# Kernel tuning notes

Measured on AMD Instinct MI355X. Metric: run time of the kernel, lower is better.

The kernel has to match this reference:

```python
import jax, jax.numpy as jnp
import numpy as np

N_NODES = 50000
N_EDGES = 800000
IN_DIM = 256
OUT_DIM = 64


def setup_inputs() -> dict:
    key = jax.random.key(0)
    k1, k2, k3, k4, k5 = jax.random.split(key, 5)
    h = jax.random.normal(k1, (N_NODES, IN_DIM), dtype=jnp.float32)
    # fc: Linear(in_dim, out_dim, bias=False) -> weight shape [out_dim, in_dim]
    W_fc = jax.random.normal(k2, (OUT_DIM, IN_DIM), dtype=jnp.float32) / np.sqrt(IN_DIM)
    # attn_fc: Linear(2*out_dim, 1, bias=False) -> weight shape [1, 2*out_dim]
    W_attn = jax.random.normal(k3, (1, 2 * OUT_DIM), dtype=jnp.float32) / np.sqrt(2 * OUT_DIM)
    src = jax.random.randint(k4, (N_EDGES,), 0, N_NODES, dtype=jnp.int64 if jax.config.read('jax_enable_x64') else jnp.int32).astype(jnp.int32)
    dst = jax.random.randint(k5, (N_EDGES,), 0, N_NODES, dtype=jnp.int32)
    return {"h": h, "W_fc": W_fc, "W_attn": W_attn, "src": src, "dst": dst}


def reference(h, W_fc, W_attn, src, dst):
    # z = self.fc(h)
    z = h @ W_fc.T                              # [N, D]
    # edge_attention: e = leaky_relu(attn_fc(cat(z_src, z_dst)))
    z_src = z[src]                              # [E, D] gather
    z_dst = z[dst]                              # [E, D] gather
    z2 = jnp.concatenate([z_src, z_dst], axis=1)  # [E, 2D]
    e = jax.nn.leaky_relu(z2 @ W_attn.T)[:, 0]  # [E], torch default slope 0.01
    # reduce_func: segment softmax over incoming edges per dst node
    n = h.shape[0]
    m = jax.ops.segment_max(e, dst, num_segments=n)        # [N] per-node max
    e_exp = jnp.exp(e - m[dst])                             # [E] stable exp
    denom = jax.ops.segment_sum(e_exp, dst, num_segments=n)  # [N]
    alpha = e_exp / jnp.maximum(denom, 1e-16)[dst]          # [E]
    # h' = sum_j alpha_ij * z_j
    out = jax.ops.segment_sum(alpha[:, None] * z_src, dst, num_segments=n)  # [N, D]
    return out
```

## Files before the change

kernel.cpp:

```cpp
#include <hip/hip_runtime.h>

#define N_NODES 50000
#define N_EDGES 800000
#define IN_DIM  256
#define OUT_DIM 64
#define BINW    128
#define NBINS   512
#define NBINS_USED ((N_NODES + BINW - 1) / BINW)
#define PB      112
#define CH4     ((N_EDGES / 4 + PB - 1) / PB)
#define NB_GEMM ((N_NODES + 63) / 64)
#define GRID_FUSED 896

typedef _Float16 f16;
typedef __attribute__((ext_vector_type(2))) __fp16 hf16x2;
typedef __attribute__((ext_vector_type(4))) _Float16 f16x4;
typedef __attribute__((ext_vector_type(8))) _Float16 f16x8;
typedef __attribute__((ext_vector_type(4))) float f32x4;

__device__ __forceinline__ unsigned int pack_sw(int s, float w) {
    f16 hw = (f16)w;
    unsigned short us;
    __builtin_memcpy(&us, &hw, 2);
    return ((unsigned int)s << 16) | us;
}
__device__ __forceinline__ float unpack_w(unsigned int e) {
    unsigned short us = (unsigned short)(e & 0xffffu);
    f16 hw;
    __builtin_memcpy(&hw, &us, 2);
    return (float)hw;
}


__global__ __launch_bounds__(256) void k_prep(const float* __restrict__ W,
                                              f16* __restrict__ Wh,
                                              int* __restrict__ binCount) {
    int idx = blockIdx.x * 256 + threadIdx.x;
    if (idx < (OUT_DIM * IN_DIM) / 4) {
        float4 v = ((const float4*)W)[idx];
        f16x4 p = { (f16)v.x, (f16)v.y, (f16)v.z, (f16)v.w };
        ((f16x4*)Wh)[idx] = p;
    }
    if (idx < NBINS) binCount[idx] = 0;
}

__global__ __launch_bounds__(256) void k_fused(const float* __restrict__ h,
                                               const f16* __restrict__ Wh,
                                               const float* __restrict__ Wa,
                                               const int* __restrict__ dst,
                                               f16* __restrict__ z,
                                               float* __restrict__ a_src,
                                               float* __restrict__ a_dst,
                                               int* __restrict__ binCount,
                                               int* __restrict__ base) {
    __shared__ int hist[NBINS];
    const int g = blockIdx.x;
    const int t = threadIdx.x;

    if ((g & 7) == 7) {
        const int pb = g >> 3;
        for (int b = t; b < NBINS; b += 256) hist[b] = 0;
        __syncthreads();
        const int s4 = pb * CH4;
        const int e4 = min(s4 + CH4, N_EDGES / 4);
        for (int i4 = s4 + t; i4 < e4; i4 += 256) {
            int4 dv = ((const int4*)dst)[i4];
            atomicAdd(&hist[dv.x >> 7], 1);
            atomicAdd(&hist[dv.y >> 7], 1);
            atomicAdd(&hist[dv.z >> 7], 1);
            atomicAdd(&hist[dv.w >> 7], 1);
        }
        __syncthreads();
        for (int b = t; b < NBINS; b += 256) {
            int c = hist[b];
            if (c) base[pb * NBINS + b] = atomicAdd(&binCount[b], c);
        }
        return;
    }

    const int gemm_id = g - (g >> 3);
    if (gemm_id >= NB_GEMM) return;

    const int row0  = gemm_id * 64;
    const int lane  = t & 63;
    const int wid   = t >> 6;
    const int cl    = lane & 15;
    const int khalf = lane >> 4;

    int arow = row0 + wid * 16 + cl;
    if (arow >= N_NODES) arow = N_NODES - 1;
    const float* hrow = h + (size_t)arow * IN_DIM;

    f32x4 acc[4] = {};

    #pragma unroll 4
    for (int kc = 0; kc < IN_DIM; kc += 32) {
        const int k0 = kc + khalf * 8;
        float4 va = *(const float4*)&hrow[k0];
        float4 vb = *(const float4*)&hrow[k0 + 4];
        union { hf16x2 h2[4]; f16x8 h8; } ua;
        ua.h2[0] = __builtin_amdgcn_cvt_pkrtz(va.x, va.y);
        ua.h2[1] = __builtin_amdgcn_cvt_pkrtz(va.z, va.w);
        ua.h2[2] = __builtin_amdgcn_cvt_pkrtz(vb.x, vb.y);
        ua.h2[3] = __builtin_amdgcn_cvt_pkrtz(vb.z, vb.w);
        f16x8 a = ua.h8;
        #pragma unroll
        for (int ct = 0; ct < 4; ++ct) {
            const int col = ct * 16 + cl;
            f16x8 b = *(const f16x8*)&Wh[col * 256 + k0];
            acc[ct] = __builtin_amdgcn_mfma_f32_16x16x32_f16(a, b, acc[ct], 0, 0, 0);
        }
    }

    const int rbase = row0 + wid * 16 + khalf * 4;
    #pragma unroll
    for (int ct = 0; ct < 4; ++ct) {
        #pragma unroll
        for (int r = 0; r < 4; ++r) {
            int row = rbase + r;
            if (row < N_NODES)
                z[(size_t)row * OUT_DIM + ct * 16 + cl] = (f16)acc[ct][r];
        }
    }

    float wa1[4], wa2[4];
    #pragma unroll
    for (int ct = 0; ct < 4; ++ct) {
        wa1[ct] = Wa[ct * 16 + cl];
        wa2[ct] = Wa[64 + ct * 16 + cl];
    }
    #pragma unroll
    for (int r = 0; r < 4; ++r) {
        float s1 = 0.f, s2 = 0.f;
        #pragma unroll
        for (int ct = 0; ct < 4; ++ct) {
            s1 += acc[ct][r] * wa1[ct];
            s2 += acc[ct][r] * wa2[ct];
        }
        #pragma unroll
        for (int off = 1; off < 16; off <<= 1) {
            s1 += __shfl_xor(s1, off);
            s2 += __shfl_xor(s2, off);
        }
        int row = rbase + r;
        if (cl == 0 && row < N_NODES) {
            a_src[row] = s1;
            a_dst[row] = s2;
        }
    }
}

__global__ __launch_bounds__(256) void k_place(const int* __restrict__ src,
                                               const int* __restrict__ dst,
                                               const int* __restrict__ binCount,
                                               const int* __restrict__ base,
                                               int* __restrict__ ebuf) {
    __shared__ int cursor[NBINS];
    const int pb = blockIdx.x;
    const int t  = threadIdx.x;

    if (t < 64) {
        int vals[8]; int run = 0;
        #pragma unroll
        for (int i = 0; i < 8; ++i) { int c = binCount[t * 8 + i]; vals[i] = run; run += c; }
        int incl = run;
        #pragma unroll
        for (int off = 1; off < 64; off <<= 1) {
            int u = __shfl_up(incl, off);
            if (t >= off) incl += u;
        }
        const int lex = incl - run;
        #pragma unroll
        for (int i = 0; i < 8; ++i) cursor[t * 8 + i] = lex + vals[i];
    }
    __syncthreads();
    for (int b = t; b < NBINS; b += 256) cursor[b] += base[pb * NBINS + b];
    __syncthreads();

    const int s4 = pb * CH4;
    const int e4 = min(s4 + CH4, N_EDGES / 4);
    for (int i4 = s4 + t; i4 < e4; i4 += 256) {
        int4 dv = ((const int4*)dst)[i4];
        int4 sv = ((const int4*)src)[i4];
        int slot;
        slot = atomicAdd(&cursor[dv.x >> 7], 1); ebuf[slot] = (sv.x << 7) | (dv.x & 127);
        slot = atomicAdd(&cursor[dv.y >> 7], 1); ebuf[slot] = (sv.y << 7) | (dv.y & 127);
        slot = atomicAdd(&cursor[dv.z >> 7], 1); ebuf[slot] = (sv.z << 7) | (dv.z & 127);
        slot = atomicAdd(&cursor[dv.w >> 7], 1); ebuf[slot] = (sv.w << 7) | (dv.w & 127);
    }
}

__global__ __launch_bounds__(256) void k_place2(const int* __restrict__ ebuf,
                                                const int* __restrict__ binCount,
                                                const float* __restrict__ a_src,
                                                const float* __restrict__ a_dst,
                                                int* __restrict__ csr,
                                                int* __restrict__ rowptr) {
    __shared__ int cnt[BINW];
    __shared__ int cur[BINW];
    __shared__ float adl[BINW];
    __shared__ int sh_estart;
    const int b  = blockIdx.x;
    const int t  = threadIdx.x;
    const int node0 = b * BINW;
    const int ecnt  = binCount[b];

    if (t < 64) {
        int partial = 0;
        for (int i = t; i < b; i += 64) partial += binCount[i];
        #pragma unroll
        for (int off = 32; off; off >>= 1) partial += __shfl_xor(partial, off);
        if (t == 0) sh_estart = partial;
    }
    if (t < BINW) {
        cnt[t] = 0;
        int gd = node0 + t;
        adl[t] = (gd < N_NODES) ? a_dst[gd] : 0.f;
    }
    __syncthreads();
    const int estart = sh_estart;

    for (int i = t; i < ecnt; i += 256)
        atomicAdd(&cnt[ebuf[estart + i] & (BINW - 1)], 1);
    __syncthreads();

    if (t < 64) {
        int v0 = cnt[t], v1 = cnt[t + 64];
        int i0 = v0;
        #pragma unroll
        for (int off = 1; off < 64; off <<= 1) {
            int u = __shfl_up(i0, off);
            if (t >= off) i0 += u;
        }
        int tot0 = __shfl(i0, 63);
        int i1 = v1;
        #pragma unroll
        for (int off = 1; off < 64; off <<= 1) {
            int u = __shfl_up(i1, off);
            if (t >= off) i1 += u;
        }
        int e0 = i0 - v0;
        int e1 = tot0 + i1 - v1;
        cur[t]      = e0;
        cur[t + 64] = e1;
        if (node0 + t <= N_NODES)      rowptr[node0 + t]      = estart + e0;
        if (node0 + t + 64 <= N_NODES) rowptr[node0 + t + 64] = estart + e1;
    }
    __syncthreads();

    for (int i = t; i < ecnt; i += 256) {
        int pk = ebuf[estart + i];
        int ld = pk & (BINW - 1);
        int s  = pk >> 7;
        float u = a_src[s] + adl[ld];
        u = u > 0.f ? u : 0.01f * u;
        float w = __expf(u);
        int p  = atomicAdd(&cur[ld], 1);
        csr[estart + p] = (int)pack_sw(s, w);
    }
}

__global__ __launch_bounds__(256) void k_aggregate(const int* __restrict__ rowptr,
                                                   const int* __restrict__ csr,
                                                   const float* __restrict__ a_src,
                                                   const float* __restrict__ a_dst,
                                                   const f16* __restrict__ z,
                                                   float* __restrict__ out) {
    __shared__ unsigned int buf[4][64];
    const int wid  = threadIdx.x >> 6;
    const int lane = threadIdx.x & 63;
    const int node = blockIdx.x * 4 + wid;
    if (node >= N_NODES) return;

    const int beg = rowptr[node];
    const int end = rowptr[node + 1];
    const int deg = end - beg;

    const int grp = lane >> 3;
    const int cl  = lane & 7;
    float dn = 0.0f;
    float acc8[8] = {0.f, 0.f, 0.f, 0.f, 0.f, 0.f, 0.f, 0.f};

    if (deg <= 64) {
        unsigned int e = 0;
        if (lane < deg) e = (unsigned int)csr[beg + lane];
        dn = unpack_w(e);

        buf[wid][lane] = e;
        __builtin_amdgcn_wave_barrier();

        const int kmax = (deg + 7) & ~7;
        for (int k = 0; k < kmax; k += 8) {
            unsigned int pe = buf[wid][k + grp];
            int   sk = (int)(pe >> 16);
            float wk = unpack_w(pe);
            f16x8 zv = *(const f16x8*)&z[(size_t)sk * OUT_DIM + cl * 8];
            #pragma unroll
            for (int j = 0; j < 8; ++j)
                acc8[j] = fmaf(wk, (float)zv[j], acc8[j]);
        }
    } else {
        const float adst = a_dst[node];
        float mx = -INFINITY;
        for (int j = beg + lane; j < end; j += 64) {
            int s = (int)(((unsigned int)csr[j]) >> 16);
            float u = a_src[s] + adst;
            u = u > 0.0f ? u : 0.01f * u;
            mx = fmaxf(mx, u);
        }
        #pragma unroll
        for (int off = 32; off; off >>= 1) mx = fmaxf(mx, __shfl_xor(mx, off));

        for (int base_ = beg; base_ < end; base_ += 64) {
            int rem = end - base_; if (rem > 64) rem = 64;
            int s = 0; float w = 0.0f;
            if (lane < rem) {
                s = (int)(((unsigned int)csr[base_ + lane]) >> 16);
                float u = a_src[s] + adst;
                u = u > 0.0f ? u : 0.01f * u;
                w = __expf(u - mx);
            }
            dn += w;
            __builtin_amdgcn_wave_barrier();
            buf[wid][lane] = pack_sw(s, w);
            __builtin_amdgcn_wave_barrier();

            const int kmax = (rem + 7) & ~7;
            for (int k = 0; k < kmax; k += 8) {
                unsigned int pe = buf[wid][k + grp];
                int   sk = (int)(pe >> 16);
                float wk = unpack_w(pe);
                f16x8 zv = *(const f16x8*)&z[(size_t)sk * OUT_DIM + cl * 8];
                #pragma unroll
                for (int j = 0; j < 8; ++j)
                    acc8[j] = fmaf(wk, (float)zv[j], acc8[j]);
            }
            __builtin_amdgcn_wave_barrier();
        }
    }

    #pragma unroll
    for (int off = 32; off; off >>= 1) dn += __shfl_xor(dn, off);
    #pragma unroll
    for (int off = 8; off < 64; off <<= 1) {
        #pragma unroll
        for (int j = 0; j < 8; ++j)
            acc8[j] += __shfl_xor(acc8[j], off);
    }

    if (lane < 8) {
        float inv = 1.0f / fmaxf(dn, 1e-16f);
        float4 o0 = make_float4(acc8[0] * inv, acc8[1] * inv, acc8[2] * inv, acc8[3] * inv);
        float4 o1 = make_float4(acc8[4] * inv, acc8[5] * inv, acc8[6] * inv, acc8[7] * inv);
        *(float4*)&out[(size_t)node * OUT_DIM + lane * 8]     = o0;
        *(float4*)&out[(size_t)node * OUT_DIM + lane * 8 + 4] = o1;
    }
}


extern "C" void kernel_launch(void* const* d_in, const int* in_sizes, int n_in,
                              void* d_out, int out_size, void* d_ws, size_t ws_size,
                              hipStream_t stream) {
    const float* h      = (const float*)d_in[0];
    const float* W_fc   = (const float*)d_in[1];
    const float* W_attn = (const float*)d_in[2];
    const int*   src    = (const int*)d_in[3];
    const int*   dst    = (const int*)d_in[4];
    float* out = (float*)d_out;

    f16*   z        = (f16*)d_ws;
    f16*   Wh       = z + (size_t)N_NODES * OUT_DIM;
    float* a_src    = (float*)(Wh + OUT_DIM * IN_DIM);
    float* a_dst    = a_src + N_NODES;
    int*   binCount = (int*)(a_dst + N_NODES);
    int*   rowptr   = binCount + NBINS;
    int*   base     = rowptr + (N_NODES + 1);
    int*   ebuf     = base + PB * NBINS;
    int*   csr      = ebuf + N_EDGES;

    k_prep<<<16, 256, 0, stream>>>(W_fc, Wh, binCount);
    k_fused<<<GRID_FUSED, 256, 0, stream>>>(h, Wh, W_attn, dst, z, a_src, a_dst, binCount, base);
    k_place<<<PB, 256, 0, stream>>>(src, dst, binCount, base, ebuf);
    k_place2<<<NBINS_USED, 256, 0, stream>>>(ebuf, binCount, a_src, a_dst, csr, rowptr);
    k_aggregate<<<(N_NODES + 3) / 4, 256, 0, stream>>>(rowptr, csr, a_src, a_dst, z, out);
}
```

Before: 80.03 us.

## Drop prep kernel: convert weights inline and derive bin offsets from per-block histograms

Removes the k_prep launch. The GEMM now reads fp32 weights directly and converts them to fp16 in registers. The global binCount atomics are replaced by per-block histogram writes, and k_place recomputes per-bin totals and prefix offsets by summing all block histograms, then publishes bin start and total arrays for k_place2. This saves one kernel launch and the atomics, at the cost of redundant weight conversion in every GEMM block and each place block reading 112x512 histogram entries.

Result: slower. 95.31 us (+19.1%).

```diff
diff --git a/kernel.cpp b/kernel.cpp
--- a/kernel.cpp
+++ b/kernel.cpp
@@ -32,26 +32,13 @@
 }
 
 
-__global__ __launch_bounds__(256) void k_prep(const float* __restrict__ W,
-                                              f16* __restrict__ Wh,
-                                              int* __restrict__ binCount) {
-    int idx = blockIdx.x * 256 + threadIdx.x;
-    if (idx < (OUT_DIM * IN_DIM) / 4) {
-        float4 v = ((const float4*)W)[idx];
-        f16x4 p = { (f16)v.x, (f16)v.y, (f16)v.z, (f16)v.w };
-        ((f16x4*)Wh)[idx] = p;
-    }
-    if (idx < NBINS) binCount[idx] = 0;
-}
-
 __global__ __launch_bounds__(256) void k_fused(const float* __restrict__ h,
-                                               const f16* __restrict__ Wh,
+                                               const float* __restrict__ W,
                                                const float* __restrict__ Wa,
                                                const int* __restrict__ dst,
                                                f16* __restrict__ z,
                                                float* __restrict__ a_src,
                                                float* __restrict__ a_dst,
-                                               int* __restrict__ binCount,
                                                int* __restrict__ base) {
     __shared__ int hist[NBINS];
     const int g = blockIdx.x;
@@ -71,10 +58,8 @@
             atomicAdd(&hist[dv.w >> 7], 1);
         }
         __syncthreads();
-        for (int b = t; b < NBINS; b += 256) {
-            int c = hist[b];
-            if (c) base[pb * NBINS + b] = atomicAdd(&binCount[b], c);
-        }
+        for (int b = t; b < NBINS; b += 256)
+            base[pb * NBINS + b] = hist[b];
         return;
     }
 
@@ -107,8 +92,15 @@
         #pragma unroll
         for (int ct = 0; ct < 4; ++ct) {
             const int col = ct * 16 + cl;
-            f16x8 b = *(const f16x8*)&Wh[col * 256 + k0];
-            acc[ct] = __builtin_amdgcn_mfma_f32_16x16x32_f16(a, b, acc[ct], 0, 0, 0);
+            const float* wrow = W + (size_t)col * IN_DIM;
+            float4 wa4 = *(const float4*)&wrow[k0];
+            float4 wb4 = *(const float4*)&wrow[k0 + 4];
+            union { hf16x2 h2[4]; f16x8 h8; } ub;
+            ub.h2[0] = __builtin_amdgcn_cvt_pkrtz(wa4.x, wa4.y);
+            ub.h2[1] = __builtin_amdgcn_cvt_pkrtz(wa4.z, wa4.w);
+            ub.h2[2] = __builtin_amdgcn_cvt_pkrtz(wb4.x, wb4.y);
+            ub.h2[3] = __builtin_amdgcn_cvt_pkrtz(wb4.z, wb4.w);
+            acc[ct] = __builtin_amdgcn_mfma_f32_16x16x32_f16(a, ub.h8, acc[ct], 0, 0, 0);
         }
     }
 
@@ -152,17 +144,34 @@
 
 __global__ __launch_bounds__(256) void k_place(const int* __restrict__ src,
                                                const int* __restrict__ dst,
-                                               const int* __restrict__ binCount,
                                                const int* __restrict__ base,
+                                               int* __restrict__ binStartG,
+                                               int* __restrict__ binTotalG,
                                                int* __restrict__ ebuf) {
     __shared__ int cursor[NBINS];
+    __shared__ int totalL[NBINS];
+    __shared__ int bstart[NBINS];
     const int pb = blockIdx.x;
     const int t  = threadIdx.x;
 
+    int myPre[2];
+    #pragma unroll
+    for (int i = 0; i < 2; ++i) {
+        const int b = t + i * 256;
+        int total = 0, pre = 0;
+        for (int q = 0; q < PB; ++q) {
+            int v = base[q * NBINS + b];
+            total += v;
+            if (q < pb) pre += v;
+        }
+        totalL[b] = total;
+        myPre[i] = pre;
+    }
+    __syncthreads();
     if (t < 64) {
         int vals[8]; int run = 0;
         #pragma unroll
-        for (int i = 0; i < 8; ++i) { int c = binCount[t * 8 + i]; vals[i] = run; run += c; }
+        for (int i = 0; i < 8; ++i) { int c = totalL[t * 8 + i]; vals[i] = run; run += c; }
         int incl = run;
         #pragma unroll
         for (int off = 1; off < 64; off <<= 1) {
@@ -171,10 +180,18 @@
         }
         const int lex = incl - run;
         #pragma unroll
-        for (int i = 0; i < 8; ++i) cursor[t * 8 + i] = lex + vals[i];
-    }
-    __syncthreads();
-    for (int b = t; b < NBINS; b += 256) cursor[b] += base[pb * NBINS + b];
+        for (int i = 0; i < 8; ++i) bstart[t * 8 + i] = lex + vals[i];
+    }
+    __syncthreads();
+    #pragma unroll
+    for (int i = 0; i < 2; ++i) {
+        const int b = t + i * 256;
+        cursor[b] = bstart[b] + myPre[i];
+        if (pb == 0) {
+            binStartG[b] = bstart[b];
+            binTotalG[b] = totalL[b];
+        }
+    }
     __syncthreads();
 
     const int s4 = pb * CH4;
@@ -191,7 +208,8 @@
 }
 
 __global__ __launch_bounds__(256) void k_place2(const int* __restrict__ ebuf,
-                                                const int* __restrict__ binCount,
+                                                const int* __restrict__ binStartG,
+                                                const int* __restrict__ binTotalG,
                                                 const float* __restrict__ a_src,
                                                 const float* __restrict__ a_dst,
                                                 int* __restrict__ csr,
@@ -199,26 +217,18 @@
     __shared__ int cnt[BINW];
     __shared__ int cur[BINW];
     __shared__ float adl[BINW];
-    __shared__ int sh_estart;
     const int b  = blockIdx.x;
     const int t  = threadIdx.x;
-    const int node0 = b * BINW;
-    const int ecnt  = binCount[b];
-
-    if (t < 64) {
-        int partial = 0;
-        for (int i = t; i < b; i += 64) partial += binCount[i];
-        #pragma unroll
-        for (int off = 32; off; off >>= 1) partial += __shfl_xor(partial, off);
-        if (t == 0) sh_estart = partial;
-    }
+    const int node0  = b * BINW;
+    const int estart = binStartG[b];
+    const int ecnt   = binTotalG[b];
+
     if (t < BINW) {
         cnt[t] = 0;
         int gd = node0 + t;
         adl[t] = (gd < N_NODES) ? a_dst[gd] : 0.f;
     }
     __syncthreads();
-    const int estart = sh_estart;
 
     for (int i = t; i < ecnt; i += 256)
         atomicAdd(&cnt[ebuf[estart + i] & (BINW - 1)], 1);
@@ -369,18 +379,17 @@
     float* out = (float*)d_out;
 
     f16*   z        = (f16*)d_ws;
-    f16*   Wh       = z + (size_t)N_NODES * OUT_DIM;
-    float* a_src    = (float*)(Wh + OUT_DIM * IN_DIM);
+    float* a_src    = (float*)(z + (size_t)N_NODES * OUT_DIM);
     float* a_dst    = a_src + N_NODES;
-    int*   binCount = (int*)(a_dst + N_NODES);
-    int*   rowptr   = binCount + NBINS;
-    int*   base     = rowptr + (N_NODES + 1);
-    int*   ebuf     = base + PB * NBINS;
+    int*   base     = (int*)(a_dst + N_NODES);
+    int*   binStartG= base + PB * NBINS;
+    int*   binTotalG= binStartG + NBINS;
+    int*   rowptr   = binTotalG + NBINS;
+    int*   ebuf     = rowptr + (N_NODES + 1);
     int*   csr      = ebuf + N_EDGES;
 
-    k_prep<<<16, 256, 0, stream>>>(W_fc, Wh, binCount);
-    k_fused<<<GRID_FUSED, 256, 0, stream>>>(h, Wh, W_attn, dst, z, a_src, a_dst, binCount, base);
-    k_place<<<PB, 256, 0, stream>>>(src, dst, binCount, base, ebuf);
-    k_place2<<<NBINS_USED, 256, 0, stream>>>(ebuf, binCount, a_src, a_dst, csr, rowptr);
+    k_fused<<<GRID_FUSED, 256, 0, stream>>>(h, W_fc, W_attn, dst, z, a_src, a_dst, base);
+    k_place<<<PB, 256, 0, stream>>>(src, dst, base, binStartG, binTotalG, ebuf);
+    k_place2<<<NBINS_USED, 256, 0, stream>>>(ebuf, binStartG, binTotalG, a_src, a_dst, csr, rowptr);
     k_aggregate<<<(N_NODES + 3) / 4, 256, 0, stream>>>(rowptr, csr, a_src, a_dst, z, out);
 }
```

## Fuse CSR placement and aggregation into one per-bin kernel using LDS CSR

Applied to the files above, without the earlier changes.

Merges k_place2 and k_aggregate into one kernel, k_binagg, with one 1024-thread block per 128-node bin. Each block builds that bin's packed (src, weight) CSR in shared memory and then aggregates its nodes directly, 8 nodes per wave. This removes the global csr and rowptr writes and reads and one kernel launch. In exchange it launches far fewer waves, each handling several nodes in sequence, so less gather latency can be hidden. It also drops the max-subtracted path for high-degree nodes and silently truncates any bin with more than 4096 edges.

After: 79.94 us. About the same (-0.1%).

```diff
diff --git a/kernel.cpp b/kernel.cpp
--- a/kernel.cpp
+++ b/kernel.cpp
@@ -11,6 +11,7 @@
 #define CH4     ((N_EDGES / 4 + PB - 1) / PB)
 #define NB_GEMM ((N_NODES + 63) / 64)
 #define GRID_FUSED 896
+#define CSRCAP  4096
 
 typedef _Float16 f16;
 typedef __attribute__((ext_vector_type(2))) __fp16 hf16x2;
@@ -190,20 +191,24 @@
     }
 }
 
-__global__ __launch_bounds__(256) void k_place2(const int* __restrict__ ebuf,
-                                                const int* __restrict__ binCount,
-                                                const float* __restrict__ a_src,
-                                                const float* __restrict__ a_dst,
-                                                int* __restrict__ csr,
-                                                int* __restrict__ rowptr) {
+__global__ __launch_bounds__(1024) void k_binagg(const int* __restrict__ ebuf,
+                                                 const int* __restrict__ binCount,
+                                                 const float* __restrict__ a_src,
+                                                 const float* __restrict__ a_dst,
+                                                 const f16* __restrict__ z,
+                                                 float* __restrict__ out) {
     __shared__ int cnt[BINW];
+    __shared__ int rb[BINW];
     __shared__ int cur[BINW];
     __shared__ float adl[BINW];
+    __shared__ unsigned int lcsr[CSRCAP];
     __shared__ int sh_estart;
-    const int b  = blockIdx.x;
-    const int t  = threadIdx.x;
+    const int b    = blockIdx.x;
+    const int t    = threadIdx.x;
+    const int lane = t & 63;
+    const int wid  = t >> 6;
     const int node0 = b * BINW;
-    const int ecnt  = binCount[b];
+    const int ecnt  = min(binCount[b], CSRCAP);
 
     if (t < 64) {
         int partial = 0;
@@ -220,7 +225,7 @@
     __syncthreads();
     const int estart = sh_estart;
 
-    for (int i = t; i < ecnt; i += 256)
+    for (int i = t; i < ecnt; i += 1024)
         atomicAdd(&cnt[ebuf[estart + i] & (BINW - 1)], 1);
     __syncthreads();
 
@@ -241,93 +246,43 @@
         }
         int e0 = i0 - v0;
         int e1 = tot0 + i1 - v1;
-        cur[t]      = e0;
-        cur[t + 64] = e1;
-        if (node0 + t <= N_NODES)      rowptr[node0 + t]      = estart + e0;
-        if (node0 + t + 64 <= N_NODES) rowptr[node0 + t + 64] = estart + e1;
-    }
-    __syncthreads();
-
-    for (int i = t; i < ecnt; i += 256) {
+        rb[t]       = e0;  cur[t]      = e0;
+        rb[t + 64]  = e1;  cur[t + 64] = e1;
+    }
+    __syncthreads();
+
+    for (int i = t; i < ecnt; i += 1024) {
         int pk = ebuf[estart + i];
         int ld = pk & (BINW - 1);
         int s  = pk >> 7;
         float u = a_src[s] + adl[ld];
         u = u > 0.f ? u : 0.01f * u;
         float w = __expf(u);
-        int p  = atomicAdd(&cur[ld], 1);
-        csr[estart + p] = (int)pack_sw(s, w);
-    }
-}
-
-__global__ __launch_bounds__(256) void k_aggregate(const int* __restrict__ rowptr,
-                                                   const int* __restrict__ csr,
-                                                   const float* __restrict__ a_src,
-                                                   const float* __restrict__ a_dst,
-                                                   const f16* __restrict__ z,
-                                                   float* __restrict__ out) {
-    __shared__ unsigned int buf[4][64];
-    const int wid  = threadIdx.x >> 6;
-    const int lane = threadIdx.x & 63;
-    const int node = blockIdx.x * 4 + wid;
-    if (node >= N_NODES) return;
-
-    const int beg = rowptr[node];
-    const int end = rowptr[node + 1];
-    const int deg = end - beg;
+        int p = atomicAdd(&cur[ld], 1);
+        lcsr[p] = pack_sw(s, w);
+    }
+    __syncthreads();
 
     const int grp = lane >> 3;
     const int cl  = lane & 7;
-    float dn = 0.0f;
-    float acc8[8] = {0.f, 0.f, 0.f, 0.f, 0.f, 0.f, 0.f, 0.f};
-
-    if (deg <= 64) {
-        unsigned int e = 0;
-        if (lane < deg) e = (unsigned int)csr[beg + lane];
-        dn = unpack_w(e);
-
-        buf[wid][lane] = e;
-        __builtin_amdgcn_wave_barrier();
-
-        const int kmax = (deg + 7) & ~7;
-        for (int k = 0; k < kmax; k += 8) {
-            unsigned int pe = buf[wid][k + grp];
-            int   sk = (int)(pe >> 16);
-            float wk = unpack_w(pe);
-            f16x8 zv = *(const f16x8*)&z[(size_t)sk * OUT_DIM + cl * 8];
-            #pragma unroll
-            for (int j = 0; j < 8; ++j)
-                acc8[j] = fmaf(wk, (float)zv[j], acc8[j]);
-        }
-    } else {
-        const float adst = a_dst[node];
-        float mx = -INFINITY;
-        for (int j = beg + lane; j < end; j += 64) {
-            int s = (int)(((unsigned int)csr[j]) >> 16);
-            float u = a_src[s] + adst;
-            u = u > 0.0f ? u : 0.01f * u;
-            mx = fmaxf(mx, u);
-        }
-        #pragma unroll
-        for (int off = 32; off; off >>= 1) mx = fmaxf(mx, __shfl_xor(mx, off));
-
-        for (int base_ = beg; base_ < end; base_ += 64) {
-            int rem = end - base_; if (rem > 64) rem = 64;
-            int s = 0; float w = 0.0f;
-            if (lane < rem) {
-                s = (int)(((unsigned int)csr[base_ + lane]) >> 16);
-                float u = a_src[s] + adst;
-                u = u > 0.0f ? u : 0.01f * u;
-                w = __expf(u - mx);
-            }
-            dn += w;
-            __builtin_amdgcn_wave_barrier();
-            buf[wid][lane] = pack_sw(s, w);
-            __builtin_amdgcn_wave_barrier();
-
+    #pragma unroll
+    for (int i = 0; i < 8; ++i) {
+        const int ld   = i * 16 + wid;
+        const int node = node0 + ld;
+        if (node >= N_NODES) continue;
+        const int beg = rb[ld];
+        const int deg = cnt[ld];
+
+        float dn = 0.0f;
+        float acc8[8] = {0.f, 0.f, 0.f, 0.f, 0.f, 0.f, 0.f, 0.f};
+
+        for (int cb = 0; cb < deg; cb += 64) {
+            const int rem = min(deg - cb, 64);
+            if (lane < rem) dn += unpack_w(lcsr[beg + cb + lane]);
             const int kmax = (rem + 7) & ~7;
             for (int k = 0; k < kmax; k += 8) {
-                unsigned int pe = buf[wid][k + grp];
+                const int ei = k + grp;
+                unsigned int pe = (ei < rem) ? lcsr[beg + cb + ei] : 0u;
                 int   sk = (int)(pe >> 16);
                 float wk = unpack_w(pe);
                 f16x8 zv = *(const f16x8*)&z[(size_t)sk * OUT_DIM + cl * 8];
@@ -335,25 +290,24 @@
                 for (int j = 0; j < 8; ++j)
                     acc8[j] = fmaf(wk, (float)zv[j], acc8[j]);
             }
-            __builtin_amdgcn_wave_barrier();
-        }
-    }
-
-    #pragma unroll
-    for (int off = 32; off; off >>= 1) dn += __shfl_xor(dn, off);
-    #pragma unroll
-    for (int off = 8; off < 64; off <<= 1) {
-        #pragma unroll
-        for (int j = 0; j < 8; ++j)
-            acc8[j] += __shfl_xor(acc8[j], off);
-    }
-
-    if (lane < 8) {
-        float inv = 1.0f / fmaxf(dn, 1e-16f);
-        float4 o0 = make_float4(acc8[0] * inv, acc8[1] * inv, acc8[2] * inv, acc8[3] * inv);
-        float4 o1 = make_float4(acc8[4] * inv, acc8[5] * inv, acc8[6] * inv, acc8[7] * inv);
-        *(float4*)&out[(size_t)node * OUT_DIM + lane * 8]     = o0;
-        *(float4*)&out[(size_t)node * OUT_DIM + lane * 8 + 4] = o1;
+        }
+
+        #pragma unroll
+        for (int off = 32; off; off >>= 1) dn += __shfl_xor(dn, off);
+        #pragma unroll
+        for (int off = 8; off < 64; off <<= 1) {
+            #pragma unroll
+            for (int j = 0; j < 8; ++j)
+                acc8[j] += __shfl_xor(acc8[j], off);
+        }
+
+        if (lane < 8) {
+            float inv = 1.0f / fmaxf(dn, 1e-16f);
+            float4 o0 = make_float4(acc8[0] * inv, acc8[1] * inv, acc8[2] * inv, acc8[3] * inv);
+            float4 o1 = make_float4(acc8[4] * inv, acc8[5] * inv, acc8[6] * inv, acc8[7] * inv);
+            *(float4*)&out[(size_t)node * OUT_DIM + lane * 8]     = o0;
+            *(float4*)&out[(size_t)node * OUT_DIM + lane * 8 + 4] = o1;
+        }
     }
 }
 
@@ -373,14 +327,11 @@
     float* a_src    = (float*)(Wh + OUT_DIM * IN_DIM);
     float* a_dst    = a_src + N_NODES;
     int*   binCount = (int*)(a_dst + N_NODES);
-    int*   rowptr   = binCount + NBINS;
-    int*   base     = rowptr + (N_NODES + 1);
+    int*   base     = binCount + NBINS;
     int*   ebuf     = base + PB * NBINS;
-    int*   csr      = ebuf + N_EDGES;
 
     k_prep<<<16, 256, 0, stream>>>(W_fc, Wh, binCount);
     k_fused<<<GRID_FUSED, 256, 0, stream>>>(h, Wh, W_attn, dst, z, a_src, a_dst, binCount, base);
     k_place<<<PB, 256, 0, stream>>>(src, dst, binCount, base, ebuf);
-    k_place2<<<NBINS_USED, 256, 0, stream>>>(ebuf, binCount, a_src, a_dst, csr, rowptr);
-    k_aggregate<<<(N_NODES + 3) / 4, 256, 0, stream>>>(rowptr, csr, a_src, a_dst, z, out);
-}
+    k_binagg<<<NBINS_USED, 1024, 0, stream>>>(ebuf, binCount, a_src, a_dst, z, out);
+}
```
